# Kernel tuning notes

Hardware: AMD Instinct MI355X
Metric: run time of the kernel (lower is better)

## Reference

```python
import jax, jax.numpy as jnp
import numpy as np

STRIDES = (8, 16, 32)
FEAT_SIZES = ((80, 80), (40, 40), (20, 20))  # (h, w) per level for 640x640 input
OFFSET = 0.5
NMS_K = 300
IOU_THR = 0.65
EPS = 1e-7


def make_priors():
    """MlvlPointGenerator.grid_priors with with_stride=True, flattened over levels."""
    pts, strs = [], []
    for (h, w), s in zip(FEAT_SIZES, STRIDES):
        xs = (jnp.arange(w, dtype=jnp.float32) + OFFSET) * s
        ys = (jnp.arange(h, dtype=jnp.float32) + OFFSET) * s
        yy, xx = jnp.meshgrid(ys, xs, indexing='ij')
        pts.append(jnp.stack([xx.reshape(-1), yy.reshape(-1)], -1))
        strs.append(jnp.full((h * w, 2), float(s), dtype=jnp.float32))
    return jnp.concatenate(pts, 0), jnp.concatenate(strs, 0)  # [N,2], [N,2]


def pairwise_iou(boxes):  # boxes [K,4] xyxy
    area = jnp.clip(boxes[:, 2] - boxes[:, 0], 0) * jnp.clip(boxes[:, 3] - boxes[:, 1], 0)
    lt = jnp.maximum(boxes[:, None, :2], boxes[None, :, :2])
    rb = jnp.minimum(boxes[:, None, 2:], boxes[None, :, 2:])
    wh = jnp.clip(rb - lt, 0)
    inter = wh[..., 0] * wh[..., 1]
    union = area[:, None] + area[None, :] - inter
    return inter / (union + EPS)


def nms_keep(boxes):  # boxes [K,4] sorted by descending score -> bool keep mask [K]
    K = boxes.shape[0]
    iou = pairwise_iou(boxes)
    idx = jnp.arange(K)

    def body(i, keep):
        sup = (iou[i] > IOU_THR) & (idx > i) & keep[i]
        return keep & ~sup

    return jax.lax.fori_loop(0, K, body, jnp.ones((K,), dtype=bool))


def setup_inputs() -> dict:
    key = jax.random.key(0)
    k1, k2, k3, k4, k5 = jax.random.split(key, 5)
    B, N, K = 128, 8400, 17
    return {
        'cls_scores': jax.random.normal(k1, (B, N, 1), jnp.float32),
        'bbox_preds': jax.random.normal(k2, (B, N, 4), jnp.float32),
        'objectness': jax.random.normal(k3, (B, N), jnp.float32),
        'kpt_offsets': jax.random.normal(k4, (B, N, K, 2), jnp.float32),
        'kpt_vis_preds': jax.random.normal(k5, (B, N, K), jnp.float32),
    }


def reference(cls_scores, bbox_preds, objectness, kpt_offsets, kpt_vis_preds):
    priors, strides = make_priors()  # [N,2] each
    # bbox decode: center-offset + exp wh, YOLOX style
    xy = bbox_preds[..., :2] * strides + priors            # [B,N,2]
    wh = jnp.exp(bbox_preds[..., 2:4]) * strides           # [B,N,2]
    boxes = jnp.concatenate([xy - wh * 0.5, xy + wh * 0.5], -1)  # [B,N,4]
    scores = jax.nn.sigmoid(cls_scores[..., 0]) * jax.nn.sigmoid(objectness)  # [B,N]
    # keypoint decode
    kpts = kpt_offsets * strides[:, None, :] + priors[:, None, :]  # [B,N,K,2]
    B, N, K, _ = kpts.shape
    kpts_flat = kpts.reshape(B, N, K * 2)
    vis = jax.nn.sigmoid(kpt_vis_preds)                    # [B,N,K]
    # fixed-size top-k pre-NMS selection
    top_vals, top_idx = jax.lax.top_k(scores, NMS_K)       # [B,NMS_K]
    gather = lambda x: jnp.take_along_axis(x, top_idx[..., None], axis=1)
    boxes_k = gather(boxes)       # [B,NMS_K,4]
    kpts_k = gather(kpts_flat)    # [B,NMS_K,2K]
    vis_k = gather(vis)           # [B,NMS_K,K]
    keep = jax.vmap(nms_keep)(boxes_k)                      # [B,NMS_K] bool
    final_scores = top_vals * keep.astype(top_vals.dtype)
    # [B, NMS_K, 4 + 1 + 2K + K]
    return jnp.concatenate([boxes_k, final_scores[..., None], kpts_k, vis_k], -1)
```

## Files before the change

### kernel.cpp

```cpp
#include <hip/hip_runtime.h>
#include <math.h>

#define BATCH 128
#define NANCH 8400
#define NMSK  300
#define KPT   17
#define OUTC  56
#define CAND  1024
#define NTHR  1024
#define NBIN  8192
#define BSHIFT 19

__device__ __forceinline__ void prior_of(int i, float& stride, float& cx, float& cy) {
    int row, col;
    if (i < 6400)      { stride = 8.0f;  row = i / 80;              col = i - row * 80; }
    else if (i < 8000) { int ii = i - 6400; stride = 16.0f; row = ii / 40; col = ii - row * 40; }
    else               { int ii = i - 8000; stride = 32.0f; row = ii / 20; col = ii - row * 20; }
    cx = ((float)col + 0.5f) * stride;
    cy = ((float)row + 0.5f) * stride;
}

__global__ __launch_bounds__(NTHR) void fused_kernel(
    const float* __restrict__ cls, const float* __restrict__ obj,
    const float* __restrict__ bbox, const float* __restrict__ kofs,
    const float* __restrict__ kvis, float* __restrict__ out)
{
    const int b    = blockIdx.x >> 1;
    const int role = blockIdx.x & 1;
    const int tid  = threadIdx.x;
    const int lane = tid & 63;
    const int wv   = tid >> 6;

    __shared__ __align__(16) unsigned int sc[NANCH];
    __shared__ __align__(16) unsigned int hist[NBIN];
    __shared__ unsigned int wtot[16], wab[16];
    __shared__ unsigned int sh_pivot, sh_cnt;
    __shared__ unsigned long long ckey[CAND];
    __shared__ float bx1[NMSK], by1[NMSK], bx2[NMSK], by2[NMSK], area[NMSK];
    __shared__ float sval[NMSK], pst[NMSK], ppx[NMSK], ppy[NMSK];
    __shared__ int   sidx[NMSK];
    __shared__ unsigned long long supl[NMSK * 6];
    __shared__ unsigned long long keepw[5];

    {
        const float4* c4 = (const float4*)(cls + (size_t)b * NANCH);
        const float4* o4 = (const float4*)(obj + (size_t)b * NANCH);
        for (int i = tid; i < NANCH / 4; i += NTHR) {
            float4 cv = c4[i];
            float4 ov = o4[i];
            float sa0 = 1.0f / (1.0f + (float)exp(-(double)cv.x));
            float sa1 = 1.0f / (1.0f + (float)exp(-(double)cv.y));
            float sa2 = 1.0f / (1.0f + (float)exp(-(double)cv.z));
            float sa3 = 1.0f / (1.0f + (float)exp(-(double)cv.w));
            float so0 = 1.0f / (1.0f + (float)exp(-(double)ov.x));
            float so1 = 1.0f / (1.0f + (float)exp(-(double)ov.y));
            float so2 = 1.0f / (1.0f + (float)exp(-(double)ov.z));
            float so3 = 1.0f / (1.0f + (float)exp(-(double)ov.w));
            sc[4 * i + 0] = __float_as_uint(sa0 * so0);
            sc[4 * i + 1] = __float_as_uint(sa1 * so1);
            sc[4 * i + 2] = __float_as_uint(sa2 * so2);
            sc[4 * i + 3] = __float_as_uint(sa3 * so3);
        }
        uint4 z; z.x = z.y = z.z = z.w = 0u;
        uint4* h4 = (uint4*)hist;
        for (int i = tid; i < NBIN / 4; i += NTHR) h4[i] = z;
        if (tid == 0) sh_cnt = 0u;
    }
    __syncthreads();

    for (int i = tid; i < NANCH; i += NTHR) atomicAdd(&hist[sc[i] >> BSHIFT], 1u);
    __syncthreads();

    unsigned int s7[8];
    {
        uint4 a = ((uint4*)hist)[2 * tid];
        uint4 c = ((uint4*)hist)[2 * tid + 1];
        unsigned int h0 = a.x, h1 = a.y, h2 = a.z, h3 = a.w;
        unsigned int h4 = c.x, h5 = c.y, h6 = c.z, h7 = c.w;
        s7[7] = h7;
        s7[6] = s7[7] + h6; s7[5] = s7[6] + h5; s7[4] = s7[5] + h4;
        s7[3] = s7[4] + h3; s7[2] = s7[3] + h2; s7[1] = s7[2] + h1;
        s7[0] = s7[1] + h0;
    }
    unsigned int T = s7[0];
    unsigned int v = T;
    #pragma unroll
    for (int d = 1; d < 64; d <<= 1) {
        unsigned int t2 = (unsigned int)__shfl_down((int)v, d, 64);
        if (lane + d < 64) v += t2;
    }
    unsigned int aiw = v - T;
    if (lane == 0) wtot[wv] = v;
    __syncthreads();
    if (tid < 16) {
        unsigned int wa = 0;
        for (int q = tid + 1; q < 16; ++q) wa += wtot[q];
        wab[tid] = wa;
    }
    __syncthreads();
    {
        unsigned int ag = wab[wv] + aiw;
        #pragma unroll
        for (int k = 0; k < 8; ++k) hist[8 * tid + k] = ag + s7[k];
    }
    __syncthreads();

    #pragma unroll
    for (int k = 0; k < 8; ++k) {
        unsigned int bin = 8 * (unsigned)tid + k;
        unsigned int ge = hist[bin];
        unsigned int gn = (bin < NBIN - 1) ? hist[bin + 1] : 0u;
        if (ge >= NMSK && gn < NMSK) sh_pivot = bin;
    }
    __syncthreads();
    unsigned int pivot_bits = sh_pivot << BSHIFT;

    for (int base = 0; base < NANCH; base += NTHR) {
        int i = base + tid;
        bool valid = (i < NANCH);
        unsigned int key = valid ? sc[i] : 0u;
        bool pred = valid && (key >= pivot_bits);
        unsigned long long m = __ballot(pred);
        unsigned int cnt = (unsigned int)__popcll(m);
        unsigned int wbase = 0u;
        if (lane == 0 && cnt) wbase = atomicAdd(&sh_cnt, cnt);
        wbase = (unsigned int)__shfl((int)wbase, 0, 64);
        if (pred) {
            unsigned int p = wbase + (unsigned int)__popcll(m & ((1ull << lane) - 1ull));
            if (p < CAND)
                ckey[p] = ((unsigned long long)key << 32)
                        | (unsigned long long)(0xFFFFFFFFu - (unsigned int)i);
        }
    }
    __syncthreads();
    unsigned int M = sh_cnt; if (M > CAND) M = CAND;

    if (tid < (int)M) {
        unsigned long long mine = ckey[tid];
        int rank = 0;
        for (unsigned int t2 = 0; t2 < M; ++t2) rank += (ckey[t2] > mine) ? 1 : 0;
        if (rank < NMSK) {
            sidx[rank] = (int)(0xFFFFFFFFu - (unsigned int)(mine & 0xFFFFFFFFull));
            sval[rank] = __uint_as_float((unsigned int)(mine >> 32));
        }
    }
    __syncthreads();

    if (role == 0) {
        if (tid < NMSK) {
            int j = tid;
            int i = sidx[j];
            float stride, cx, cy;
            prior_of(i, stride, cx, cy);
            float4 bb = *(const float4*)(bbox + ((size_t)b * NANCH + (size_t)i) * 4);
            float x = bb.x * stride + cx;
            float y = bb.y * stride + cy;
            float w = expf(bb.z) * stride;
            float h = expf(bb.w) * stride;
            float x1 = x - 0.5f * w, y1 = y - 0.5f * h;
            float x2 = x + 0.5f * w, y2 = y + 0.5f * h;
            bx1[j] = x1; by1[j] = y1; bx2[j] = x2; by2[j] = y2;
            area[j] = fmaxf(x2 - x1, 0.0f) * fmaxf(y2 - y1, 0.0f);
        }
        __syncthreads();

        for (int t = tid; t < NMSK * 5; t += NTHR) {
            int w = t / NMSK;
            int i = t - w * NMSK;
            int jlo = w * 64; if (jlo < i + 1) jlo = i + 1;
            int jhi = w * 64 + 64; if (jhi > NMSK) jhi = NMSK;
            unsigned long long m = 0;
            float ax1 = bx1[i], ay1 = by1[i], ax2 = bx2[i], ay2 = by2[i], aa = area[i];
            for (int j = jlo; j < jhi; ++j) {
                float lx = fmaxf(ax1, bx1[j]);
                float ly = fmaxf(ay1, by1[j]);
                float rx = fminf(ax2, bx2[j]);
                float ry = fminf(ay2, by2[j]);
                float iw = fmaxf(rx - lx, 0.0f);
                float ih = fmaxf(ry - ly, 0.0f);
                float inter = iw * ih;
                float iou = inter / (aa + area[j] - inter + 1e-7f);
                if (iou > 0.65f) m |= 1ull << (j & 63);
            }
            supl[i * 6 + w] = m;
        }
        __syncthreads();

        if (tid < 64) {
            int j = tid;
            unsigned long long keep0 = ~0ull, keep1 = ~0ull, keep2 = ~0ull, keep3 = ~0ull;
            unsigned long long keep4 = (1ull << (NMSK - 256)) - 1ull;
            #define CHUNK(C, KC, IMAX) { \
                int r = (C) * 64 + j; \
                unsigned int lo0=0,hi0=0,lo1=0,hi1=0,lo2=0,hi2=0,lo3=0,hi3=0,lo4=0,hi4=0; \
                if (r < NMSK) { \
                    unsigned long long w0 = supl[r*6+0], w1 = supl[r*6+1], w2 = supl[r*6+2]; \
                    unsigned long long w3 = supl[r*6+3], w4 = supl[r*6+4]; \
                    lo0=(unsigned int)w0; hi0=(unsigned int)(w0>>32); \
                    lo1=(unsigned int)w1; hi1=(unsigned int)(w1>>32); \
                    lo2=(unsigned int)w2; hi2=(unsigned int)(w2>>32); \
                    lo3=(unsigned int)w3; hi3=(unsigned int)(w3>>32); \
                    lo4=(unsigned int)w4; hi4=(unsigned int)(w4>>32); } \
                for (int bi = 0; bi < (IMAX); ++bi) { \
                    if ((KC >> bi) & 1ull) { \
                        unsigned long long s0 = ((unsigned long long)__builtin_amdgcn_readlane(hi0,bi)<<32) | __builtin_amdgcn_readlane(lo0,bi); \
                        unsigned long long s1 = ((unsigned long long)__builtin_amdgcn_readlane(hi1,bi)<<32) | __builtin_amdgcn_readlane(lo1,bi); \
                        unsigned long long s2 = ((unsigned long long)__builtin_amdgcn_readlane(hi2,bi)<<32) | __builtin_amdgcn_readlane(lo2,bi); \
                        unsigned long long s3 = ((unsigned long long)__builtin_amdgcn_readlane(hi3,bi)<<32) | __builtin_amdgcn_readlane(lo3,bi); \
                        unsigned long long s4 = ((unsigned long long)__builtin_amdgcn_readlane(hi4,bi)<<32) | __builtin_amdgcn_readlane(lo4,bi); \
                        keep0 &= ~s0; keep1 &= ~s1; keep2 &= ~s2; keep3 &= ~s3; keep4 &= ~s4; } } }
            CHUNK(0, keep0, 64)
            CHUNK(1, keep1, 64)
            CHUNK(2, keep2, 64)
            CHUNK(3, keep3, 64)
            CHUNK(4, keep4, NMSK - 256)
            #undef CHUNK
            if (j == 0) { keepw[0]=keep0; keepw[1]=keep1; keepw[2]=keep2; keepw[3]=keep3; keepw[4]=keep4; }
        } else {
            float* ob = out + (size_t)b * NMSK * OUTC;
            for (int t = tid - 64; t < NMSK * 4; t += NTHR - 64) {
                int j = t >> 2, ci = t & 3;
                float vv = (ci == 0) ? bx1[j] : (ci == 1) ? by1[j] : (ci == 2) ? bx2[j] : by2[j];
                ob[j * OUTC + ci] = vv;
            }
        }
        __syncthreads();

        if (tid < NMSK) {
            bool kp = (keepw[tid >> 6] >> (tid & 63)) & 1ull;
            out[(size_t)b * NMSK * OUTC + (size_t)tid * OUTC + 4] = kp ? sval[tid] : 0.0f;
        }
    } else {
        if (tid < NMSK) {
            int i = sidx[tid];
            float stride, cx, cy;
            prior_of(i, stride, cx, cy);
            pst[tid] = stride; ppx[tid] = cx; ppy[tid] = cy;
        }
        __syncthreads();

        const float* kof = kofs + (size_t)b * NANCH * 34;
        const float* kvi = kvis + (size_t)b * NANCH * KPT;
        float* ob = out + (size_t)b * NMSK * OUTC;
        for (int e = tid; e < NMSK * 51; e += NTHR) {
            int j  = e / 51;
            int ci = e - j * 51;
            int i  = sidx[j];
            float vv;
            if (ci < 34) {
                float off = kof[(size_t)i * 34 + ci];
                vv = off * pst[j] + ((ci & 1) ? ppy[j] : ppx[j]);
            } else {
                float x = kvi[(size_t)i * KPT + (ci - 34)];
                vv = 1.0f / (1.0f + expf(-x));
            }
            ob[j * OUTC + 5 + ci] = vv;
        }
    }
}

extern "C" void kernel_launch(void* const* d_in, const int* in_sizes, int n_in,
                              void* d_out, int out_size, void* d_ws, size_t ws_size,
                              hipStream_t stream) {
    const float* cls  = (const float*)d_in[0];
    const float* bbox = (const float*)d_in[1];
    const float* obj  = (const float*)d_in[2];
    const float* kofs = (const float*)d_in[3];
    const float* kvis = (const float*)d_in[4];
    float* out = (float*)d_out;

    (void)d_ws; (void)ws_size;

    fused_kernel<<<BATCH * 2, NTHR, 0, stream>>>(cls, obj, bbox, kofs, kvis, out);
}
```

Before: 296.6 us.

## Merge dual-role blocks into one block per image with register-held scores

Launches one block per batch image instead of two. Each block computes the scores and top-k once, then overlaps the NMS wave with keypoint gathering in the remaining waves. Scores stay in per-thread registers instead of a shared array, the prefix-sum writeback and a barrier are removed, and box decode is folded into the rank step. The aim is to stop every image's score, histogram and top-k work being done twice. The cost is half as many blocks (128 on a GPU with 256 CUs) and fewer threads left for the keypoint gather.

```diff
diff --git a/kernel.cpp b/kernel.cpp
--- a/kernel.cpp
+++ b/kernel.cpp
@@ -10,6 +10,7 @@
 #define NTHR  1024
 #define NBIN  8192
 #define BSHIFT 19
+#define NGRP  (NANCH / 4)
 
 __device__ __forceinline__ void prior_of(int i, float& stride, float& cx, float& cy) {
     int row, col;
@@ -25,62 +26,76 @@
     const float* __restrict__ bbox, const float* __restrict__ kofs,
     const float* __restrict__ kvis, float* __restrict__ out)
 {
-    const int b    = blockIdx.x >> 1;
-    const int role = blockIdx.x & 1;
+    const int b    = blockIdx.x;
     const int tid  = threadIdx.x;
     const int lane = tid & 63;
     const int wv   = tid >> 6;
 
-    __shared__ __align__(16) unsigned int sc[NANCH];
     __shared__ __align__(16) unsigned int hist[NBIN];
     __shared__ unsigned int wtot[16], wab[16];
     __shared__ unsigned int sh_pivot, sh_cnt;
     __shared__ unsigned long long ckey[CAND];
     __shared__ float bx1[NMSK], by1[NMSK], bx2[NMSK], by2[NMSK], area[NMSK];
-    __shared__ float sval[NMSK], pst[NMSK], ppx[NMSK], ppy[NMSK];
+    __shared__ float sval[NMSK];
     __shared__ int   sidx[NMSK];
     __shared__ unsigned long long supl[NMSK * 6];
     __shared__ unsigned long long keepw[5];
 
+    unsigned int sck[12];
     {
         const float4* c4 = (const float4*)(cls + (size_t)b * NANCH);
         const float4* o4 = (const float4*)(obj + (size_t)b * NANCH);
-        for (int i = tid; i < NANCH / 4; i += NTHR) {
-            float4 cv = c4[i];
-            float4 ov = o4[i];
-            float sa0 = 1.0f / (1.0f + (float)exp(-(double)cv.x));
-            float sa1 = 1.0f / (1.0f + (float)exp(-(double)cv.y));
-            float sa2 = 1.0f / (1.0f + (float)exp(-(double)cv.z));
-            float sa3 = 1.0f / (1.0f + (float)exp(-(double)cv.w));
-            float so0 = 1.0f / (1.0f + (float)exp(-(double)ov.x));
-            float so1 = 1.0f / (1.0f + (float)exp(-(double)ov.y));
-            float so2 = 1.0f / (1.0f + (float)exp(-(double)ov.z));
-            float so3 = 1.0f / (1.0f + (float)exp(-(double)ov.w));
-            sc[4 * i + 0] = __float_as_uint(sa0 * so0);
-            sc[4 * i + 1] = __float_as_uint(sa1 * so1);
-            sc[4 * i + 2] = __float_as_uint(sa2 * so2);
-            sc[4 * i + 3] = __float_as_uint(sa3 * so3);
+        #pragma unroll
+        for (int k = 0; k < 3; ++k) {
+            int g = tid + k * NTHR;
+            if (g < NGRP) {
+                float4 cv = c4[g];
+                float4 ov = o4[g];
+                float sa0 = 1.0f / (1.0f + (float)exp(-(double)cv.x));
+                float sa1 = 1.0f / (1.0f + (float)exp(-(double)cv.y));
+                float sa2 = 1.0f / (1.0f + (float)exp(-(double)cv.z));
+                float sa3 = 1.0f / (1.0f + (float)exp(-(double)cv.w));
+                float so0 = 1.0f / (1.0f + (float)exp(-(double)ov.x));
+                float so1 = 1.0f / (1.0f + (float)exp(-(double)ov.y));
+                float so2 = 1.0f / (1.0f + (float)exp(-(double)ov.z));
+                float so3 = 1.0f / (1.0f + (float)exp(-(double)ov.w));
+                sck[4 * k + 0] = __float_as_uint(sa0 * so0);
+                sck[4 * k + 1] = __float_as_uint(sa1 * so1);
+                sck[4 * k + 2] = __float_as_uint(sa2 * so2);
+                sck[4 * k + 3] = __float_as_uint(sa3 * so3);
+            } else {
+                sck[4 * k + 0] = 0u; sck[4 * k + 1] = 0u;
+                sck[4 * k + 2] = 0u; sck[4 * k + 3] = 0u;
+            }
         }
         uint4 z; z.x = z.y = z.z = z.w = 0u;
         uint4* h4 = (uint4*)hist;
-        for (int i = tid; i < NBIN / 4; i += NTHR) h4[i] = z;
+        h4[tid] = z;
+        h4[tid + NTHR] = z;
         if (tid == 0) sh_cnt = 0u;
     }
     __syncthreads();
 
-    for (int i = tid; i < NANCH; i += NTHR) atomicAdd(&hist[sc[i] >> BSHIFT], 1u);
+    #pragma unroll
+    for (int k = 0; k < 3; ++k) {
+        int g = tid + k * NTHR;
+        if (g < NGRP) {
+            atomicAdd(&hist[sck[4 * k + 0] >> BSHIFT], 1u);
+            atomicAdd(&hist[sck[4 * k + 1] >> BSHIFT], 1u);
+            atomicAdd(&hist[sck[4 * k + 2] >> BSHIFT], 1u);
+            atomicAdd(&hist[sck[4 * k + 3] >> BSHIFT], 1u);
+        }
+    }
     __syncthreads();
 
     unsigned int s7[8];
     {
         uint4 a = ((uint4*)hist)[2 * tid];
         uint4 c = ((uint4*)hist)[2 * tid + 1];
-        unsigned int h0 = a.x, h1 = a.y, h2 = a.z, h3 = a.w;
-        unsigned int h4 = c.x, h5 = c.y, h6 = c.z, h7 = c.w;
-        s7[7] = h7;
-        s7[6] = s7[7] + h6; s7[5] = s7[6] + h5; s7[4] = s7[5] + h4;
-        s7[3] = s7[4] + h3; s7[2] = s7[3] + h2; s7[1] = s7[2] + h1;
-        s7[0] = s7[1] + h0;
+        s7[7] = c.w;
+        s7[6] = s7[7] + c.z; s7[5] = s7[6] + c.y; s7[4] = s7[5] + c.x;
+        s7[3] = s7[4] + a.w; s7[2] = s7[3] + a.z; s7[1] = s7[2] + a.y;
+        s7[0] = s7[1] + a.x;
     }
     unsigned int T = s7[0];
     unsigned int v = T;
@@ -98,38 +113,39 @@
         wab[tid] = wa;
     }
     __syncthreads();
+
     {
         unsigned int ag = wab[wv] + aiw;
         #pragma unroll
-        for (int k = 0; k < 8; ++k) hist[8 * tid + k] = ag + s7[k];
-    }
-    __syncthreads();
+        for (int k = 0; k < 8; ++k) {
+            unsigned int ge = ag + s7[k];
+            unsigned int gn = (k < 7) ? (ag + s7[k + 1]) : ag;
+            if (ge >= NMSK && gn < NMSK) sh_pivot = 8u * (unsigned)tid + (unsigned)k;
+        }
+    }
+    __syncthreads();
+    unsigned int pivot_bits = sh_pivot << BSHIFT;
 
     #pragma unroll
-    for (int k = 0; k < 8; ++k) {
-        unsigned int bin = 8 * (unsigned)tid + k;
-        unsigned int ge = hist[bin];
-        unsigned int gn = (bin < NBIN - 1) ? hist[bin + 1] : 0u;
-        if (ge >= NMSK && gn < NMSK) sh_pivot = bin;
-    }
-    __syncthreads();
-    unsigned int pivot_bits = sh_pivot << BSHIFT;
-
-    for (int base = 0; base < NANCH; base += NTHR) {
-        int i = base + tid;
-        bool valid = (i < NANCH);
-        unsigned int key = valid ? sc[i] : 0u;
-        bool pred = valid && (key >= pivot_bits);
-        unsigned long long m = __ballot(pred);
-        unsigned int cnt = (unsigned int)__popcll(m);
-        unsigned int wbase = 0u;
-        if (lane == 0 && cnt) wbase = atomicAdd(&sh_cnt, cnt);
-        wbase = (unsigned int)__shfl((int)wbase, 0, 64);
-        if (pred) {
-            unsigned int p = wbase + (unsigned int)__popcll(m & ((1ull << lane) - 1ull));
-            if (p < CAND)
-                ckey[p] = ((unsigned long long)key << 32)
-                        | (unsigned long long)(0xFFFFFFFFu - (unsigned int)i);
+    for (int k = 0; k < 3; ++k) {
+        int g = tid + k * NTHR;
+        bool valid = (g < NGRP);
+        #pragma unroll
+        for (int s = 0; s < 4; ++s) {
+            unsigned int key = sck[4 * k + s];
+            bool pred = valid && (key >= pivot_bits);
+            unsigned long long m = __ballot(pred);
+            unsigned int cnt = (unsigned int)__popcll(m);
+            unsigned int wbase = 0u;
+            if (lane == 0 && cnt) wbase = atomicAdd(&sh_cnt, cnt);
+            wbase = (unsigned int)__shfl((int)wbase, 0, 64);
+            if (pred) {
+                unsigned int p = wbase + (unsigned int)__popcll(m & ((1ull << lane) - 1ull));
+                unsigned int idx = 4u * (unsigned)g + (unsigned)s;
+                if (p < CAND)
+                    ckey[p] = ((unsigned long long)key << 32)
+                            | (unsigned long long)(0xFFFFFFFFu - idx);
+            }
         }
     }
     __syncthreads();
@@ -140,16 +156,9 @@
         int rank = 0;
         for (unsigned int t2 = 0; t2 < M; ++t2) rank += (ckey[t2] > mine) ? 1 : 0;
         if (rank < NMSK) {
-            sidx[rank] = (int)(0xFFFFFFFFu - (unsigned int)(mine & 0xFFFFFFFFull));
+            int i = (int)(0xFFFFFFFFu - (unsigned int)(mine & 0xFFFFFFFFull));
+            sidx[rank] = i;
             sval[rank] = __uint_as_float((unsigned int)(mine >> 32));
-        }
-    }
-    __syncthreads();
-
-    if (role == 0) {
-        if (tid < NMSK) {
-            int j = tid;
-            int i = sidx[j];
             float stride, cx, cy;
             prior_of(i, stride, cx, cy);
             float4 bb = *(const float4*)(bbox + ((size_t)b * NANCH + (size_t)i) * 4);
@@ -159,103 +168,96 @@
             float h = expf(bb.w) * stride;
             float x1 = x - 0.5f * w, y1 = y - 0.5f * h;
             float x2 = x + 0.5f * w, y2 = y + 0.5f * h;
-            bx1[j] = x1; by1[j] = y1; bx2[j] = x2; by2[j] = y2;
-            area[j] = fmaxf(x2 - x1, 0.0f) * fmaxf(y2 - y1, 0.0f);
-        }
-        __syncthreads();
-
-        for (int t = tid; t < NMSK * 5; t += NTHR) {
-            int w = t / NMSK;
-            int i = t - w * NMSK;
-            int jlo = w * 64; if (jlo < i + 1) jlo = i + 1;
-            int jhi = w * 64 + 64; if (jhi > NMSK) jhi = NMSK;
-            unsigned long long m = 0;
-            float ax1 = bx1[i], ay1 = by1[i], ax2 = bx2[i], ay2 = by2[i], aa = area[i];
-            for (int j = jlo; j < jhi; ++j) {
-                float lx = fmaxf(ax1, bx1[j]);
-                float ly = fmaxf(ay1, by1[j]);
-                float rx = fminf(ax2, bx2[j]);
-                float ry = fminf(ay2, by2[j]);
-                float iw = fmaxf(rx - lx, 0.0f);
-                float ih = fmaxf(ry - ly, 0.0f);
-                float inter = iw * ih;
-                float iou = inter / (aa + area[j] - inter + 1e-7f);
-                if (iou > 0.65f) m |= 1ull << (j & 63);
-            }
-            supl[i * 6 + w] = m;
-        }
-        __syncthreads();
-
-        if (tid < 64) {
-            int j = tid;
-            unsigned long long keep0 = ~0ull, keep1 = ~0ull, keep2 = ~0ull, keep3 = ~0ull;
-            unsigned long long keep4 = (1ull << (NMSK - 256)) - 1ull;
-            #define CHUNK(C, KC, IMAX) { \
-                int r = (C) * 64 + j; \
-                unsigned int lo0=0,hi0=0,lo1=0,hi1=0,lo2=0,hi2=0,lo3=0,hi3=0,lo4=0,hi4=0; \
-                if (r < NMSK) { \
-                    unsigned long long w0 = supl[r*6+0], w1 = supl[r*6+1], w2 = supl[r*6+2]; \
-                    unsigned long long w3 = supl[r*6+3], w4 = supl[r*6+4]; \
-                    lo0=(unsigned int)w0; hi0=(unsigned int)(w0>>32); \
-                    lo1=(unsigned int)w1; hi1=(unsigned int)(w1>>32); \
-                    lo2=(unsigned int)w2; hi2=(unsigned int)(w2>>32); \
-                    lo3=(unsigned int)w3; hi3=(unsigned int)(w3>>32); \
-                    lo4=(unsigned int)w4; hi4=(unsigned int)(w4>>32); } \
-                for (int bi = 0; bi < (IMAX); ++bi) { \
-                    if ((KC >> bi) & 1ull) { \
-                        unsigned long long s0 = ((unsigned long long)__builtin_amdgcn_readlane(hi0,bi)<<32) | __builtin_amdgcn_readlane(lo0,bi); \
-                        unsigned long long s1 = ((unsigned long long)__builtin_amdgcn_readlane(hi1,bi)<<32) | __builtin_amdgcn_readlane(lo1,bi); \
-                        unsigned long long s2 = ((unsigned long long)__builtin_amdgcn_readlane(hi2,bi)<<32) | __builtin_amdgcn_readlane(lo2,bi); \
-                        unsigned long long s3 = ((unsigned long long)__builtin_amdgcn_readlane(hi3,bi)<<32) | __builtin_amdgcn_readlane(lo3,bi); \
-                        unsigned long long s4 = ((unsigned long long)__builtin_amdgcn_readlane(hi4,bi)<<32) | __builtin_amdgcn_readlane(lo4,bi); \
-                        keep0 &= ~s0; keep1 &= ~s1; keep2 &= ~s2; keep3 &= ~s3; keep4 &= ~s4; } } }
-            CHUNK(0, keep0, 64)
-            CHUNK(1, keep1, 64)
-            CHUNK(2, keep2, 64)
-            CHUNK(3, keep3, 64)
-            CHUNK(4, keep4, NMSK - 256)
-            #undef CHUNK
-            if (j == 0) { keepw[0]=keep0; keepw[1]=keep1; keepw[2]=keep2; keepw[3]=keep3; keepw[4]=keep4; }
-        } else {
-            float* ob = out + (size_t)b * NMSK * OUTC;
-            for (int t = tid - 64; t < NMSK * 4; t += NTHR - 64) {
-                int j = t >> 2, ci = t & 3;
-                float vv = (ci == 0) ? bx1[j] : (ci == 1) ? by1[j] : (ci == 2) ? bx2[j] : by2[j];
-                ob[j * OUTC + ci] = vv;
-            }
-        }
-        __syncthreads();
-
-        if (tid < NMSK) {
-            bool kp = (keepw[tid >> 6] >> (tid & 63)) & 1ull;
-            out[(size_t)b * NMSK * OUTC + (size_t)tid * OUTC + 4] = kp ? sval[tid] : 0.0f;
-        }
+            bx1[rank] = x1; by1[rank] = y1; bx2[rank] = x2; by2[rank] = y2;
+            area[rank] = fmaxf(x2 - x1, 0.0f) * fmaxf(y2 - y1, 0.0f);
+        }
+    }
+    __syncthreads();
+
+    for (int t = tid; t < NMSK * 5; t += NTHR) {
+        int w = t / NMSK;
+        int i = t - w * NMSK;
+        int jlo = w * 64; if (jlo < i + 1) jlo = i + 1;
+        int jhi = w * 64 + 64; if (jhi > NMSK) jhi = NMSK;
+        unsigned long long m = 0;
+        float ax1 = bx1[i], ay1 = by1[i], ax2 = bx2[i], ay2 = by2[i], aa = area[i];
+        for (int j = jlo; j < jhi; ++j) {
+            float lx = fmaxf(ax1, bx1[j]);
+            float ly = fmaxf(ay1, by1[j]);
+            float rx = fminf(ax2, bx2[j]);
+            float ry = fminf(ay2, by2[j]);
+            float iw = fmaxf(rx - lx, 0.0f);
+            float ih = fmaxf(ry - ly, 0.0f);
+            float inter = iw * ih;
+            float iou = inter / (aa + area[j] - inter + 1e-7f);
+            if (iou > 0.65f) m |= 1ull << (j & 63);
+        }
+        supl[i * 6 + w] = m;
+    }
+    __syncthreads();
+
+    if (tid < 64) {
+        int j = tid;
+        unsigned long long keep0 = ~0ull, keep1 = ~0ull, keep2 = ~0ull, keep3 = ~0ull;
+        unsigned long long keep4 = (1ull << (NMSK - 256)) - 1ull;
+        #define CHUNK(C, KC, IMAX) { \
+            int r = (C) * 64 + j; \
+            unsigned int lo0=0,hi0=0,lo1=0,hi1=0,lo2=0,hi2=0,lo3=0,hi3=0,lo4=0,hi4=0; \
+            if (r < NMSK) { \
+                unsigned long long w0 = supl[r*6+0], w1 = supl[r*6+1], w2 = supl[r*6+2]; \
+                unsigned long long w3 = supl[r*6+3], w4 = supl[r*6+4]; \
+                lo0=(unsigned int)w0; hi0=(unsigned int)(w0>>32); \
+                lo1=(unsigned int)w1; hi1=(unsigned int)(w1>>32); \
+                lo2=(unsigned int)w2; hi2=(unsigned int)(w2>>32); \
+                lo3=(unsigned int)w3; hi3=(unsigned int)(w3>>32); \
+                lo4=(unsigned int)w4; hi4=(unsigned int)(w4>>32); } \
+            _Pragma("clang loop unroll(disable)") \
+            for (int bi = 0; bi < (IMAX); ++bi) { \
+                if ((KC >> bi) & 1ull) { \
+                    unsigned long long s0 = ((unsigned long long)__builtin_amdgcn_readlane(hi0,bi)<<32) | __builtin_amdgcn_readlane(lo0,bi); \
+                    unsigned long long s1 = ((unsigned long long)__builtin_amdgcn_readlane(hi1,bi)<<32) | __builtin_amdgcn_readlane(lo1,bi); \
+                    unsigned long long s2 = ((unsigned long long)__builtin_amdgcn_readlane(hi2,bi)<<32) | __builtin_amdgcn_readlane(lo2,bi); \
+                    unsigned long long s3 = ((unsigned long long)__builtin_amdgcn_readlane(hi3,bi)<<32) | __builtin_amdgcn_readlane(lo3,bi); \
+                    unsigned long long s4 = ((unsigned long long)__builtin_amdgcn_readlane(hi4,bi)<<32) | __builtin_amdgcn_readlane(lo4,bi); \
+                    keep0 &= ~s0; keep1 &= ~s1; keep2 &= ~s2; keep3 &= ~s3; keep4 &= ~s4; } } }
+        CHUNK(0, keep0, 64)
+        CHUNK(1, keep1, 64)
+        CHUNK(2, keep2, 64)
+        CHUNK(3, keep3, 64)
+        CHUNK(4, keep4, NMSK - 256)
+        #undef CHUNK
+        if (j == 0) { keepw[0]=keep0; keepw[1]=keep1; keepw[2]=keep2; keepw[3]=keep3; keepw[4]=keep4; }
     } else {
-        if (tid < NMSK) {
-            int i = sidx[tid];
-            float stride, cx, cy;
-            prior_of(i, stride, cx, cy);
-            pst[tid] = stride; ppx[tid] = cx; ppy[tid] = cy;
-        }
-        __syncthreads();
-
         const float* kof = kofs + (size_t)b * NANCH * 34;
         const float* kvi = kvis + (size_t)b * NANCH * KPT;
         float* ob = out + (size_t)b * NMSK * OUTC;
-        for (int e = tid; e < NMSK * 51; e += NTHR) {
+        for (int t = tid - 64; t < NMSK * 4; t += NTHR - 64) {
+            int j = t >> 2, ci = t & 3;
+            float vv = (ci == 0) ? bx1[j] : (ci == 1) ? by1[j] : (ci == 2) ? bx2[j] : by2[j];
+            ob[j * OUTC + ci] = vv;
+        }
+        for (int e = tid - 64; e < NMSK * 51; e += NTHR - 64) {
             int j  = e / 51;
             int ci = e - j * 51;
             int i  = sidx[j];
             float vv;
             if (ci < 34) {
+                float stride, cx, cy;
+                prior_of(i, stride, cx, cy);
                 float off = kof[(size_t)i * 34 + ci];
-                vv = off * pst[j] + ((ci & 1) ? ppy[j] : ppx[j]);
+                vv = off * stride + ((ci & 1) ? cy : cx);
             } else {
                 float x = kvi[(size_t)i * KPT + (ci - 34)];
                 vv = 1.0f / (1.0f + expf(-x));
             }
             ob[j * OUTC + 5 + ci] = vv;
         }
+    }
+    __syncthreads();
+
+    if (tid < NMSK) {
+        bool kp = (keepw[tid >> 6] >> (tid & 63)) & 1ull;
+        out[(size_t)b * NMSK * OUTC + (size_t)tid * OUTC + 4] = kp ? sval[tid] : 0.0f;
     }
 }
 
@@ -271,5 +273,5 @@
 
     (void)d_ws; (void)ws_size;
 
-    fused_kernel<<<BATCH * 2, NTHR, 0, stream>>>(cls, obj, bbox, kofs, kvis, out);
+    fused_kernel<<<BATCH, NTHR, 0, stream>>>(cls, obj, bbox, kofs, kvis, out);
 }
```

Result: no change. 296.2 us (-0.1%).
